# Kernel tuning notes

Hardware: AMD Instinct MI355X
Metric: run time of the kernel (lower is better)

Reference implementation:

```python
import jax, jax.numpy as jnp
import numpy as np

DIM_IN, DIM_OUT, DIM_INNER = 1024, 1024, 128
SCALE = DIM_INNER ** -0.5


def setup_inputs() -> dict:
    key = jax.random.key(0)
    k1, k2, k3, k4 = jax.random.split(key, 4)
    x = jax.random.normal(k1, (4, 4096, DIM_IN), dtype=jnp.float32)
    # torch nn.Linear stores weight as [out, in]; we keep that layout and transpose in matmul
    w_qkv = jax.random.normal(k2, (3 * DIM_INNER, DIM_IN), dtype=jnp.float32) * (DIM_IN ** -0.5)
    w_out = jax.random.normal(k3, (DIM_OUT, DIM_INNER), dtype=jnp.float32) * (DIM_INNER ** -0.5)
    b_out = jax.random.normal(k4, (DIM_OUT,), dtype=jnp.float32) * 0.02
    return {"x": x, "w_qkv": w_qkv, "w_out": w_out, "b_out": b_out}


def reference(x, w_qkv, w_out, b_out):
    # qkv projection (no bias)
    qkv = jnp.einsum('bnd,ed->bne', x, w_qkv)            # [b, n, 3*dim_inner]
    q, k, v = jnp.split(qkv, 3, axis=-1)                 # each [b, n, dim_inner]
    sim = jnp.einsum('bid,bjd->bij', q, k) * SCALE       # [b, n, n]
    n = sim.shape[-1]
    causal = jnp.triu(jnp.ones((n, n), dtype=bool), 1)   # True above diagonal
    neg = jnp.finfo(q.dtype).max
    sim = jnp.where(causal[None, :, :], -neg, sim)
    attn = jax.nn.softmax(sim, axis=-1)
    out = jnp.einsum('bij,bjd->bid', attn, v)            # [b, n, dim_inner]
    return jnp.einsum('bnd,od->bno', out, w_out) + b_out # [b, n, dim_out]
```

## Files before the change

kernel.cpp:

```cpp
#include <hip/hip_runtime.h>
#include <math.h>


typedef __attribute__((ext_vector_type(8))) short bf16x8;
typedef __attribute__((ext_vector_type(4))) short bf16x4;
typedef __attribute__((ext_vector_type(4))) float f32x4;

#define FA_SCL2 0.12751886525137387f

__device__ __forceinline__ unsigned short f2bf(float f) {
    __bf16 h = (__bf16)f;
    return __builtin_bit_cast(unsigned short, h);
}
__device__ __forceinline__ float bf2f(unsigned short h) {
    union { unsigned u; float f; } v; v.u = ((unsigned)h) << 16;
    return v.f;
}
__device__ __forceinline__ f32x4 mfma16(bf16x8 a, bf16x8 b, f32x4 c) {
    return __builtin_amdgcn_mfma_f32_16x16x32_bf16(a, b, c, 0, 0, 0);
}
__device__ __forceinline__ void gl2lds16(const void* g, void* l) {
    __builtin_amdgcn_global_load_lds(
        (const __attribute__((address_space(1))) unsigned int*)g,
        (__attribute__((address_space(3))) unsigned int*)l, 16, 0, 0);
}
__device__ __forceinline__ f32x4 vmax4(f32x4 a, f32x4 b) {
    return f32x4{fmaxf(a[0], b[0]), fmaxf(a[1], b[1]),
                 fmaxf(a[2], b[2]), fmaxf(a[3], b[3])};
}

__global__ __launch_bounds__(256)
void wcast(const float* __restrict__ W, unsigned short* __restrict__ wfm)
{
    const int idx = blockIdx.x * 256 + threadIdx.x;
    const int kc = idx & 127, r = idx >> 7;
    const float* g = W + (size_t)r * 1024 + kc * 8;
    float4 w0 = *(const float4*)g, w1 = *(const float4*)(g + 4);
    bf16x8 p;
    p[0] = (short)f2bf(w0.x); p[1] = (short)f2bf(w0.y);
    p[2] = (short)f2bf(w0.z); p[3] = (short)f2bf(w0.w);
    p[4] = (short)f2bf(w1.x); p[5] = (short)f2bf(w1.y);
    p[6] = (short)f2bf(w1.z); p[7] = (short)f2bf(w1.w);
    *(bf16x8*)&wfm[(size_t)(kc * 384 + r) * 8] = p;
}

__global__ __launch_bounds__(256)
void woutcast(const float* __restrict__ W, unsigned short* __restrict__ wofm)
{
    const int idx = blockIdx.x * 256 + threadIdx.x;
    const int c = idx & 15, rg = idx >> 4;
    const float* g = W + (size_t)rg * 128 + c * 8;
    float4 w0 = *(const float4*)g, w1 = *(const float4*)(g + 4);
    bf16x8 p;
    p[0] = (short)f2bf(w0.x); p[1] = (short)f2bf(w0.y);
    p[2] = (short)f2bf(w0.z); p[3] = (short)f2bf(w0.w);
    p[4] = (short)f2bf(w1.x); p[5] = (short)f2bf(w1.y);
    p[6] = (short)f2bf(w1.z); p[7] = (short)f2bf(w1.w);
    *(bf16x8*)&wofm[((size_t)((rg >> 6) * 16 + c) * 64 + (rg & 63)) * 8] = p;
}

__global__ __launch_bounds__(256, 3)
void gemm_qkv(const float* __restrict__ X, const unsigned short* __restrict__ Wfm,
              unsigned short* __restrict__ qfm, unsigned short* __restrict__ kfm,
              unsigned short* __restrict__ vfm)
{
    __shared__ unsigned short Asl[4096];
    __shared__ unsigned short Bsl[2][8192];
    const int tid = threadIdx.x;
    const int wv = tid >> 6, lane = tid & 63;
    const int lm = lane & 15, quad = lane >> 4;
    const int mt = blockIdx.x & 255;
    const int nt = blockIdx.x >> 8;
    const int mb = mt * 64, nb = nt * 128;
    const int wr = wv >> 1, wc = wv & 1;

    const int arow = tid >> 3, af8 = tid & 7;
    const float* gxr = X + (size_t)(mb + arow) * 1024 + af8 * 8;
    const int sg0 = (af8 * 64 + (arow ^ af8)) * 8;
    const int sg1 = sg0 + 32 * 8;

    f32x4 acc[2][4];
    #pragma unroll
    for (int i = 0; i < 2; ++i)
        #pragma unroll
        for (int j = 0; j < 4; ++j) acc[i][j] = f32x4{0.f, 0.f, 0.f, 0.f};

    auto loadA = [&](int it, float4& r0, float4& r1, float4& r2, float4& r3) {
        const float* g = gxr + it * 64;
        r0 = *(const float4*)g;
        r1 = *(const float4*)(g + 4);
        r2 = *(const float4*)(g + 32 * 1024);
        r3 = *(const float4*)(g + 32 * 1024 + 4);
    };
    auto stageA = [&](const float4& r0, const float4& r1,
                      const float4& r2, const float4& r3) {
        bf16x8 p0, p1;
        p0[0] = (short)f2bf(r0.x); p0[1] = (short)f2bf(r0.y);
        p0[2] = (short)f2bf(r0.z); p0[3] = (short)f2bf(r0.w);
        p0[4] = (short)f2bf(r1.x); p0[5] = (short)f2bf(r1.y);
        p0[6] = (short)f2bf(r1.z); p0[7] = (short)f2bf(r1.w);
        *(bf16x8*)&Asl[sg0] = p0;
        p1[0] = (short)f2bf(r2.x); p1[1] = (short)f2bf(r2.y);
        p1[2] = (short)f2bf(r2.z); p1[3] = (short)f2bf(r2.w);
        p1[4] = (short)f2bf(r3.x); p1[5] = (short)f2bf(r3.y);
        p1[6] = (short)f2bf(r3.z); p1[7] = (short)f2bf(r3.w);
        *(bf16x8*)&Asl[sg1] = p1;
    };
    auto issueB = [&](int it, int buf) {
        #pragma unroll
        for (int i = 0; i < 4; ++i) {
            const int p = wv * 4 + i;
            const int kc = p >> 1, colh = (p & 1) * 64;
            gl2lds16(Wfm + ((size_t)(it * 8 + kc) * 384 + nb + colh + lane) * 8,
                     &Bsl[buf][(kc * 128 + colh) * 8]);
        }
    };

    float4 a0, a1, a2, a3, b0, b1, b2, b3;
    loadA(0, a0, a1, a2, a3);
    issueB(0, 0);
    loadA(1, b0, b1, b2, b3);

    auto step = [&](const int i, float4& r0, float4& r1, float4& r2, float4& r3) {
        __builtin_amdgcn_s_barrier();
        stageA(r0, r1, r2, r3);
        if (i < 15) issueB(i + 1, (i + 1) & 1);
        if (i < 14) {
            loadA(i + 2, r0, r1, r2, r3);
            asm volatile("s_waitcnt vmcnt(12) lgkmcnt(0)" ::: "memory");
        } else if (i == 14) {
            asm volatile("s_waitcnt vmcnt(8) lgkmcnt(0)" ::: "memory");
        } else {
            asm volatile("s_waitcnt vmcnt(0) lgkmcnt(0)" ::: "memory");
        }
        __builtin_amdgcn_s_barrier();
        const unsigned short* Bc = Bsl[i & 1];
        bf16x8 af[2][2], bfr[2][4];
        #pragma unroll
        for (int s = 0; s < 2; ++s) {
            const int kc = s * 4 + quad;
            #pragma unroll
            for (int ii = 0; ii < 2; ++ii)
                af[s][ii] = *(const bf16x8*)
                    &Asl[(kc * 64 + ((wr * 32 + ii * 16 + lm) ^ kc)) * 8];
            #pragma unroll
            for (int j = 0; j < 4; ++j)
                bfr[s][j] = *(const bf16x8*)&Bc[(kc * 128 + wc * 64 + j * 16 + lm) * 8];
        }
        #pragma unroll
        for (int s = 0; s < 2; ++s)
            #pragma unroll
            for (int ii = 0; ii < 2; ++ii)
                #pragma unroll
                for (int j = 0; j < 4; ++j)
                    acc[ii][j] = mfma16(af[s][ii], bfr[s][j], acc[ii][j]);
    };

    for (int p = 0; p < 8; ++p) {
        step(2 * p,     a0, a1, a2, a3);
        step(2 * p + 1, b0, b1, b2, b3);
    }

    if (nt == 2) {
        unsigned short* T = &Bsl[0][0];
        __syncthreads();
        #pragma unroll
        for (int ii = 0; ii < 2; ++ii)
            #pragma unroll
            for (int j = 0; j < 4; ++j) {
                const int d = wc * 64 + j * 16 + lm;
                const int k0 = wr * 32 + ii * 16 + quad * 4;
                bf16x4 v;
                v[0] = (short)f2bf(acc[ii][j][0]);
                v[1] = (short)f2bf(acc[ii][j][1]);
                v[2] = (short)f2bf(acc[ii][j][2]);
                v[3] = (short)f2bf(acc[ii][j][3]);
                *(bf16x4*)&T[d * 72 + k0] = v;
            }
        __syncthreads();
        unsigned short* dst = vfm + (size_t)mt * 8192;
        #pragma unroll
        for (int t = 0; t < 4; ++t) {
            const int g = tid + t * 256;
            const int d = g & 127, c = g >> 7;
            bf16x8 x = *(const bf16x8*)&T[d * 72 + c * 8];
            *(bf16x8*)(dst + (size_t)(c * 128 + d) * 8) = x;
        }
    } else {
        unsigned short* dst = nt ? kfm : qfm;
        const float scl = nt ? 1.f : FA_SCL2;
        #pragma unroll
        for (int ii = 0; ii < 2; ++ii)
            #pragma unroll
            for (int j = 0; j < 4; ++j) {
                const int ncol = wc * 64 + j * 16 + lm;
                const size_t cb = ((size_t)mt * 16 + (ncol >> 3)) * 512 + (ncol & 7);
                #pragma unroll
                for (int r = 0; r < 4; ++r)
                    dst[cb + (size_t)(wr * 32 + ii * 16 + quad * 4 + r) * 8]
                        = f2bf(acc[ii][j][r] * scl);
            }
    }
}

__global__ __launch_bounds__(512, 4)
void flash_attn3(const unsigned short* __restrict__ Qfm, const unsigned short* __restrict__ Kfm,
                 const unsigned short* __restrict__ Vfm,
                 unsigned short* __restrict__ Opart, float* __restrict__ Ml)
{
    __shared__ unsigned short Klds[2][8192];
    __shared__ unsigned short Vlds[2][8192];
    __shared__ unsigned short Plds[8][1024];

    const int tid = threadIdx.x;
    const int wv = tid >> 6, lane = tid & 63;
    const int lm = lane & 15, quad = lane >> 4;

    const int bx = blockIdx.x;
    const int xcd = bx & 7;
    const int b   = xcd >> 1;
    const int r   = (bx >> 3) * 2 + (xcd & 1);
    const int sp  = r & 3;
    const int Qi  = (r < 64) ? (16 + (r >> 2)) : (15 - ((r - 64) >> 2));
    const int n   = 2 * Qi + 2;
    const int cnt = (n >> 2) + ((sp < (n & 3)) ? 1 : 0);
    const int ktb = sp * (n >> 2) + ((sp < (n & 3)) ? sp : (n & 3));
    const int kte = ktb + cnt;
    const int qtw = 2 * Qi + (wv >> 2);
    const int rw  = (wv & 3) * 16;

    const int qt0 = 2 * Qi;
    const size_t ob0 = (size_t)((b * 64 + qt0) * 4 + sp) * 8192;
    const size_t ob1 = ob0 + 4 * 8192;
    const int mlb0 = ((b * 64 + qt0) * 4 + sp) * 128, mlb1 = mlb0 + 512;

    if (cnt == 0) {
        bf16x8 z = {0, 0, 0, 0, 0, 0, 0, 0};
        #pragma unroll
        for (int t = 0; t < 2; ++t) {
            *(bf16x8*)&Opart[ob0 + (size_t)(tid + t * 512) * 8] = z;
            *(bf16x8*)&Opart[ob1 + (size_t)(tid + t * 512) * 8] = z;
        }
        if (tid < 64) { Ml[mlb0 + tid] = -INFINITY; Ml[mlb1 + tid] = -INFINITY; }
        else if (tid < 128) { Ml[mlb0 + tid] = 0.f; Ml[mlb1 + tid] = 0.f; }
        return;
    }

    {
        const size_t qb = (size_t)(b * 64 + qt0) * 8192;
        #pragma unroll
        for (int i = 0; i < 4; ++i) {
            const int p = wv * 4 + i;
            gl2lds16(Qfm + qb + (size_t)p * 512 + lane * 8, &Klds[0][0] + p * 512);
        }
    }
    __syncthreads();
    bf16x8 qf[4];
    {
        const unsigned short* Qt = &Klds[wv >> 2][0];
        #pragma unroll
        for (int c = 0; c < 4; ++c)
            qf[c] = *(const bf16x8*)&Qt[((c * 4 + quad) * 64 + rw + lm) * 8];
    }
    asm volatile("s_waitcnt lgkmcnt(0)" ::: "memory");
    __builtin_amdgcn_s_barrier();

    {
        const size_t kb = (size_t)(b * 64 + ktb) * 8192;
        #pragma unroll
        for (int i = 0; i < 2; ++i) {
            const int pc = wv * 2 + i;
            gl2lds16(Kfm + kb + pc * 512 + lane * 8, &Klds[0][pc * 512]);
            gl2lds16(Vfm + kb + pc * 512 + lane * 8, &Vlds[0][pc * 512]);
        }
    }

    f32x4 oacc[8];
    #pragma unroll
    for (int oc = 0; oc < 8; ++oc) oacc[oc] = f32x4{0.f, 0.f, 0.f, 0.f};
    f32x4 m4 = f32x4{-INFINITY, -INFINITY, -INFINITY, -INFINITY};
    f32x4 lacc = f32x4{0.f, 0.f, 0.f, 0.f};
    unsigned short* Pw = Plds[wv];
    const short ONE = (short)0x3F80;
    const bf16x8 ONESB = {ONE, ONE, ONE, ONE, ONE, ONE, ONE, ONE};

    for (int kt = ktb; kt < kte; ++kt) {
        const int cu = (kt - ktb) & 1;
        __builtin_amdgcn_s_barrier();
        if (kt + 1 < kte) {
            const size_t kb = (size_t)(b * 64 + kt + 1) * 8192;
            #pragma unroll
            for (int i = 0; i < 2; ++i) {
                const int pc = wv * 2 + i;
                gl2lds16(Kfm + kb + pc * 512 + lane * 8, &Klds[cu ^ 1][pc * 512]);
                gl2lds16(Vfm + kb + pc * 512 + lane * 8, &Vlds[cu ^ 1][pc * 512]);
            }
            asm volatile("s_waitcnt vmcnt(4)" ::: "memory");
        } else {
            asm volatile("s_waitcnt vmcnt(0)" ::: "memory");
        }
        __builtin_amdgcn_s_barrier();
        if (kt > qtw) continue;

        const unsigned short* Kc = &Klds[cu][0];
        const unsigned short* Vc = &Vlds[cu][0];

        f32x4 sv[4];
        __builtin_amdgcn_s_setprio(1);
        #pragma unroll
        for (int ct = 0; ct < 4; ++ct) {
            f32x4 a = f32x4{0.f, 0.f, 0.f, 0.f};
            #pragma unroll
            for (int c = 0; c < 4; ++c) {
                bf16x8 kf = *(const bf16x8*)&Kc[((c * 4 + quad) * 64 + ct * 16 + lm) * 8];
                a = mfma16(qf[c], kf, a);
            }
            sv[ct] = a;
        }
        __builtin_amdgcn_s_setprio(0);
        if (kt == qtw) {
            #pragma unroll
            for (int ct = 0; ct < 4; ++ct) {
                const int dg = ct * 16 + lm - rw - quad * 4;
                #pragma unroll
                for (int rr = 0; rr < 4; ++rr)
                    if (dg > rr) sv[ct][rr] = -INFINITY;
            }
        }
        const f32x4 pmax = vmax4(vmax4(sv[0], sv[1]), vmax4(sv[2], sv[3]));
        const float dm = fmaxf(fmaxf(pmax[0] - m4[0], pmax[1] - m4[1]),
                               fmaxf(pmax[2] - m4[2], pmax[3] - m4[3]));
        if (!__all(dm <= 8.f)) {
            f32x4 rmax = pmax;
            #pragma unroll
            for (int d = 1; d < 16; d <<= 1) {
                f32x4 o;
                #pragma unroll
                for (int e = 0; e < 4; ++e) o[e] = __shfl_xor(rmax[e], d);
                rmax = vmax4(rmax, o);
            }
            const f32x4 mnew = vmax4(m4, rmax);
            f32x4 alpha;
            #pragma unroll
            for (int e = 0; e < 4; ++e) alpha[e] = __builtin_amdgcn_exp2f(m4[e] - mnew[e]);
            m4 = mnew;
            #pragma unroll
            for (int oc = 0; oc < 8; ++oc) oacc[oc] *= alpha;
            lacc *= alpha;
        }
        #pragma unroll
        for (int ct = 0; ct < 4; ++ct)
            #pragma unroll
            for (int rr = 0; rr < 4; ++rr)
                sv[ct][rr] = __builtin_amdgcn_exp2f(sv[ct][rr] - m4[rr]);
        #pragma unroll
        for (int ct = 0; ct < 4; ++ct) {
            const int cb = ((ct * 2 + (lm >> 3)) * 16 + quad * 4) * 8 + (lm & 7);
            #pragma unroll
            for (int rr = 0; rr < 4; ++rr)
                Pw[cb + rr * 8] = f2bf(sv[ct][rr]);
        }
        __builtin_amdgcn_s_setprio(1);
        #pragma unroll
        for (int s = 0; s < 2; ++s) {
            bf16x8 pf = *(const bf16x8*)&Pw[((s * 4 + quad) * 16 + lm) * 8];
            lacc = mfma16(pf, ONESB, lacc);
            #pragma unroll
            for (int oc = 0; oc < 8; ++oc) {
                bf16x8 vf = *(const bf16x8*)&Vc[((s * 4 + quad) * 128 + oc * 16 + lm) * 8];
                oacc[oc] = mfma16(pf, vf, oacc[oc]);
            }
        }
        __builtin_amdgcn_s_setprio(0);
    }

    const size_t obw = (size_t)((b * 64 + qtw) * 4 + sp) * 8192;
    const int mlw = ((b * 64 + qtw) * 4 + sp) * 128;
    #pragma unroll
    for (int oc = 0; oc < 8; ++oc) {
        const size_t cb = obw + (size_t)((oc * 2 + (lm >> 3)) * 64
                          + rw + quad * 4) * 8 + (lm & 7);
        #pragma unroll
        for (int rr = 0; rr < 4; ++rr)
            Opart[cb + rr * 8] = f2bf(oacc[oc][rr]);
    }
    if (lm == 0)
        #pragma unroll
        for (int rr = 0; rr < 4; ++rr) {
            const int row = rw + quad * 4 + rr;
            Ml[mlw + row] = m4[rr];
            Ml[mlw + 64 + row] = lacc[rr];
        }
}

__global__ __launch_bounds__(256)
void fa_combine(const unsigned short* __restrict__ Opart, const float* __restrict__ Ml,
                unsigned short* __restrict__ Ofm)
{
    const int bq = blockIdx.x;
    const int tid = threadIdx.x;
    const size_t pbase = (size_t)bq * 4 * 8192;
    const int mlb = bq * 4 * 128;
    #pragma unroll
    for (int t = 0; t < 4; ++t) {
        const int g = tid + t * 256;
        const int r = g & 63;
        float m[4], l[4];
        #pragma unroll
        for (int s = 0; s < 4; ++s) {
            m[s] = Ml[mlb + s * 128 + r];
            l[s] = Ml[mlb + s * 128 + 64 + r];
        }
        const float M = fmaxf(fmaxf(m[0], m[1]), fmaxf(m[2], m[3]));
        float a[4], den = 0.f;
        #pragma unroll
        for (int s = 0; s < 4; ++s) {
            a[s] = __builtin_amdgcn_exp2f(m[s] - M);
            den += a[s] * l[s];
        }
        const float rsc = 1.f / den;
        float acc[8] = {};
        #pragma unroll
        for (int s = 0; s < 4; ++s) {
            bf16x8 x = *(const bf16x8*)&Opart[pbase + (size_t)s * 8192 + (size_t)g * 8];
            #pragma unroll
            for (int e = 0; e < 8; ++e) acc[e] += a[s] * bf2f((unsigned short)x[e]);
        }
        bf16x8 o;
        #pragma unroll
        for (int e = 0; e < 8; ++e) o[e] = f2bf(acc[e] * rsc);
        *(bf16x8*)&Ofm[(size_t)bq * 8192 + (size_t)g * 8] = o;
    }
}

__global__ __launch_bounds__(256, 4)
void gemm_out(const unsigned short* __restrict__ Ain, const unsigned short* __restrict__ Wofm,
              const float* __restrict__ bias, float* __restrict__ out)
{
    __shared__ unsigned short Bsl[16384];
    __shared__ unsigned short Asl[2][4096];
    const int tid = threadIdx.x;
    const int mb = blockIdx.x * 128;
    const int nb = blockIdx.y * 128;
    const int wv = tid >> 6, lane = tid & 63;
    const int wr = (wv >> 1) * 64, wc = (wv & 1) * 64;
    const int lm = lane & 15, quad = lane >> 4;

    #pragma unroll
    for (int i = 0; i < 8; ++i) {
        const int p = wv * 8 + i;
        gl2lds16(Wofm + (size_t)(((nb >> 6) + (p >> 4)) * 16 + (p & 15)) * 512 + lane * 8,
                 &Bsl[p * 512]);
    }
    #pragma unroll
    for (int i = 0; i < 2; ++i) {
        const int id = wv * 2 + i, t = id >> 2, kcl = id & 3;
        gl2lds16(Ain + (size_t)((mb >> 6) + t) * 8192 + kcl * 512 + lane * 8,
                 &Asl[0][(t * 4 + kcl) * 512]);
    }

    f32x4 acc[4][4];
    #pragma unroll
    for (int i = 0; i < 4; ++i)
        #pragma unroll
        for (int j = 0; j < 4; ++j) acc[i][j] = f32x4{0.f, 0.f, 0.f, 0.f};

    for (int kt = 0; kt < 4; ++kt) {
        __builtin_amdgcn_s_barrier();
        if (kt < 3) {
            #pragma unroll
            for (int i = 0; i < 2; ++i) {
                const int id = wv * 2 + i, t = id >> 2, kcl = id & 3;
                gl2lds16(Ain + (size_t)((mb >> 6) + t) * 8192 + ((kt + 1) * 4 + kcl) * 512 + lane * 8,
                         &Asl[(kt + 1) & 1][(t * 4 + kcl) * 512]);
            }
            asm volatile("s_waitcnt vmcnt(2)" ::: "memory");
        } else {
            asm volatile("s_waitcnt vmcnt(0)" ::: "memory");
        }
        __builtin_amdgcn_s_barrier();
        const unsigned short* Ac = Asl[kt & 1];
        bf16x8 af[4], bfr[4];
        #pragma unroll
        for (int i = 0; i < 4; ++i)
            af[i] = *(const bf16x8*)&Ac[(((wv >> 1) * 4 + quad) * 64 + i * 16 + lm) * 8];
        #pragma unroll
        for (int j = 0; j < 4; ++j)
            bfr[j] = *(const bf16x8*)&Bsl[(((wc >> 6) * 16 + kt * 4 + quad) * 64 + j * 16 + lm) * 8];
        #pragma unroll
        for (int i = 0; i < 4; ++i)
            #pragma unroll
            for (int j = 0; j < 4; ++j)
                acc[i][j] = mfma16(af[i], bfr[j], acc[i][j]);
    }

    #pragma unroll
    for (int j = 0; j < 4; ++j) {
        const int col = nb + wc + j * 16 + lm;
        const float bv = bias[col];
        #pragma unroll
        for (int i = 0; i < 4; ++i)
            #pragma unroll
            for (int r = 0; r < 4; ++r) {
                const int m = mb + wr + i * 16 + quad * 4 + r;
                out[(size_t)m * 1024 + col] = acc[i][j][r] + bv;
            }
    }
}

extern "C" void kernel_launch(void* const* d_in, const int* in_sizes, int n_in,
                              void* d_out, int out_size, void* d_ws, size_t ws_size,
                              hipStream_t stream)
{
    (void)in_sizes; (void)n_in; (void)out_size; (void)ws_size;
    const float* x     = (const float*)d_in[0];
    const float* w_qkv = (const float*)d_in[1];
    const float* w_out = (const float*)d_in[2];
    const float* b_out = (const float*)d_in[3];
    float* out = (float*)d_out;
    unsigned short* ws = (unsigned short*)d_ws;

    const size_t NE = (size_t)16384 * 128;
    unsigned short* qfm = ws;
    unsigned short* kfm = ws + NE;
    unsigned short* wofm = ws + 2 * NE;
    unsigned short* vfm = ws + 3 * NE;
    unsigned short* op  = ws + 4 * NE;
    float*          ml  = (float*)(ws + 8 * NE);
    unsigned short* ofm = qfm;
    unsigned short* wfm = op;

    hipLaunchKernelGGL(wcast,       dim3(192),    dim3(256), 0, stream, w_qkv, wfm);
    hipLaunchKernelGGL(gemm_qkv,    dim3(768),    dim3(256), 0, stream, x, wfm, qfm, kfm, vfm);
    hipLaunchKernelGGL(woutcast,    dim3(64),     dim3(256), 0, stream, w_out, wofm);
    hipLaunchKernelGGL(flash_attn3, dim3(512),    dim3(512), 0, stream, qfm, kfm, vfm, op, ml);
    hipLaunchKernelGGL(fa_combine,  dim3(256),    dim3(256), 0, stream, op, ml, ofm);
    hipLaunchKernelGGL(gemm_out,    dim3(128, 8), dim3(256), 0, stream, ofm, wofm, b_out, out);
}
```

Baseline: 181.8 us.

## Fuse split-KV combine into output GEMM and merge weight cast kernels

The flash-attention partial-result combine is folded into the output projection GEMM. Each block rescales and sums the four partial outputs for a 64-row tile straight into LDS, then loops over four 128-column tiles of W_out with double-buffered async loads. This removes the intermediate bf16 O write and read plus two kernel launches, since the two weight-cast kernels are also merged into one. In exchange, the combine work is repeated across the two column-group blocks, the grid is smaller, and LDS use per block is larger.

```diff
diff --git a/kernel.cpp b/kernel.cpp
--- a/kernel.cpp
+++ b/kernel.cpp
@@ -30,33 +30,33 @@
 }
 
 __global__ __launch_bounds__(256)
-void wcast(const float* __restrict__ W, unsigned short* __restrict__ wfm)
+void wcast_all(const float* __restrict__ Wq, const float* __restrict__ Wo,
+               unsigned short* __restrict__ wfm, unsigned short* __restrict__ wofm)
 {
-    const int idx = blockIdx.x * 256 + threadIdx.x;
-    const int kc = idx & 127, r = idx >> 7;
-    const float* g = W + (size_t)r * 1024 + kc * 8;
-    float4 w0 = *(const float4*)g, w1 = *(const float4*)(g + 4);
-    bf16x8 p;
-    p[0] = (short)f2bf(w0.x); p[1] = (short)f2bf(w0.y);
-    p[2] = (short)f2bf(w0.z); p[3] = (short)f2bf(w0.w);
-    p[4] = (short)f2bf(w1.x); p[5] = (short)f2bf(w1.y);
-    p[6] = (short)f2bf(w1.z); p[7] = (short)f2bf(w1.w);
-    *(bf16x8*)&wfm[(size_t)(kc * 384 + r) * 8] = p;
-}
-
-__global__ __launch_bounds__(256)
-void woutcast(const float* __restrict__ W, unsigned short* __restrict__ wofm)
-{
-    const int idx = blockIdx.x * 256 + threadIdx.x;
-    const int c = idx & 15, rg = idx >> 4;
-    const float* g = W + (size_t)rg * 128 + c * 8;
-    float4 w0 = *(const float4*)g, w1 = *(const float4*)(g + 4);
-    bf16x8 p;
-    p[0] = (short)f2bf(w0.x); p[1] = (short)f2bf(w0.y);
-    p[2] = (short)f2bf(w0.z); p[3] = (short)f2bf(w0.w);
-    p[4] = (short)f2bf(w1.x); p[5] = (short)f2bf(w1.y);
-    p[6] = (short)f2bf(w1.z); p[7] = (short)f2bf(w1.w);
-    *(bf16x8*)&wofm[((size_t)((rg >> 6) * 16 + c) * 64 + (rg & 63)) * 8] = p;
+    const int bx = blockIdx.x, tid = threadIdx.x;
+    if (bx < 192) {
+        const int idx = bx * 256 + tid;
+        const int kc = idx & 127, r = idx >> 7;
+        const float* g = Wq + (size_t)r * 1024 + kc * 8;
+        float4 w0 = *(const float4*)g, w1 = *(const float4*)(g + 4);
+        bf16x8 p;
+        p[0] = (short)f2bf(w0.x); p[1] = (short)f2bf(w0.y);
+        p[2] = (short)f2bf(w0.z); p[3] = (short)f2bf(w0.w);
+        p[4] = (short)f2bf(w1.x); p[5] = (short)f2bf(w1.y);
+        p[6] = (short)f2bf(w1.z); p[7] = (short)f2bf(w1.w);
+        *(bf16x8*)&wfm[(size_t)(kc * 384 + r) * 8] = p;
+    } else {
+        const int idx = (bx - 192) * 256 + tid;
+        const int c = idx & 15, rg = idx >> 4;
+        const float* g = Wo + (size_t)rg * 128 + c * 8;
+        float4 w0 = *(const float4*)g, w1 = *(const float4*)(g + 4);
+        bf16x8 p;
+        p[0] = (short)f2bf(w0.x); p[1] = (short)f2bf(w0.y);
+        p[2] = (short)f2bf(w0.z); p[3] = (short)f2bf(w0.w);
+        p[4] = (short)f2bf(w1.x); p[5] = (short)f2bf(w1.y);
+        p[6] = (short)f2bf(w1.z); p[7] = (short)f2bf(w1.w);
+        *(bf16x8*)&wofm[((size_t)((rg >> 6) * 16 + c) * 64 + (rg & 63)) * 8] = p;
+    }
 }
 
 __global__ __launch_bounds__(256, 3)
@@ -393,18 +393,33 @@
         }
 }
 
-__global__ __launch_bounds__(256)
-void fa_combine(const unsigned short* __restrict__ Opart, const float* __restrict__ Ml,
-                unsigned short* __restrict__ Ofm)
+__global__ __launch_bounds__(512, 2)
+void gemm_outf(const unsigned short* __restrict__ Opart, const float* __restrict__ Ml,
+               const unsigned short* __restrict__ Wofm, const float* __restrict__ bias,
+               float* __restrict__ out)
 {
-    const int bq = blockIdx.x;
+    __shared__ unsigned short Asl[8192];
+    __shared__ unsigned short Wl[2][16384];
     const int tid = threadIdx.x;
-    const size_t pbase = (size_t)bq * 4 * 8192;
-    const int mlb = bq * 4 * 128;
-    #pragma unroll
-    for (int t = 0; t < 4; ++t) {
-        const int g = tid + t * 256;
-        const int r = g & 63;
+    const int wv = tid >> 6, lane = tid & 63;
+    const int lm = lane & 15, quad = lane >> 4;
+    const int aq = blockIdx.x;
+    const int nt0 = blockIdx.y * 4;
+    const size_t pbase = (size_t)aq * 4 * 8192;
+    const int mlb = aq * 4 * 128;
+
+    auto issueW = [&](int nt, int buf) {
+        #pragma unroll
+        for (int i = 0; i < 4; ++i) {
+            const int p = wv * 4 + i;
+            gl2lds16(Wofm + (size_t)((nt * 2 + (p >> 4)) * 16 + (p & 15)) * 512 + lane * 8,
+                     &Wl[buf][p * 512]);
+        }
+    };
+    issueW(nt0, 0);
+
+    {
+        const int r = tid & 63;
         float m[4], l[4];
         #pragma unroll
         for (int s = 0; s < 4; ++s) {
@@ -419,92 +434,64 @@
             den += a[s] * l[s];
         }
         const float rsc = 1.f / den;
-        float acc[8] = {};
-        #pragma unroll
-        for (int s = 0; s < 4; ++s) {
-            bf16x8 x = *(const bf16x8*)&Opart[pbase + (size_t)s * 8192 + (size_t)g * 8];
-            #pragma unroll
-            for (int e = 0; e < 8; ++e) acc[e] += a[s] * bf2f((unsigned short)x[e]);
-        }
-        bf16x8 o;
-        #pragma unroll
-        for (int e = 0; e < 8; ++e) o[e] = f2bf(acc[e] * rsc);
-        *(bf16x8*)&Ofm[(size_t)bq * 8192 + (size_t)g * 8] = o;
-    }
-}
-
-__global__ __launch_bounds__(256, 4)
-void gemm_out(const unsigned short* __restrict__ Ain, const unsigned short* __restrict__ Wofm,
-              const float* __restrict__ bias, float* __restrict__ out)
-{
-    __shared__ unsigned short Bsl[16384];
-    __shared__ unsigned short Asl[2][4096];
-    const int tid = threadIdx.x;
-    const int mb = blockIdx.x * 128;
-    const int nb = blockIdx.y * 128;
-    const int wv = tid >> 6, lane = tid & 63;
-    const int wr = (wv >> 1) * 64, wc = (wv & 1) * 64;
-    const int lm = lane & 15, quad = lane >> 4;
-
+        #pragma unroll
+        for (int h = 0; h < 2; ++h) {
+            const int g = tid + h * 512;
+            float acc8[8] = {};
+            #pragma unroll
+            for (int s = 0; s < 4; ++s) {
+                bf16x8 x = *(const bf16x8*)&Opart[pbase + (size_t)s * 8192 + (size_t)g * 8];
+                #pragma unroll
+                for (int e = 0; e < 8; ++e) acc8[e] += a[s] * bf2f((unsigned short)x[e]);
+            }
+            bf16x8 o;
+            #pragma unroll
+            for (int e = 0; e < 8; ++e) o[e] = f2bf(acc8[e] * rsc);
+            *(bf16x8*)&Asl[g * 8] = o;
+        }
+    }
+    __syncthreads();
+
+    const int rw4 = (wv & 3) * 16;
+    const int tl  = wv >> 2;
+    bf16x8 af[4];
     #pragma unroll
-    for (int i = 0; i < 8; ++i) {
-        const int p = wv * 8 + i;
-        gl2lds16(Wofm + (size_t)(((nb >> 6) + (p >> 4)) * 16 + (p & 15)) * 512 + lane * 8,
-                 &Bsl[p * 512]);
-    }
-    #pragma unroll
-    for (int i = 0; i < 2; ++i) {
-        const int id = wv * 2 + i, t = id >> 2, kcl = id & 3;
-        gl2lds16(Ain + (size_t)((mb >> 6) + t) * 8192 + kcl * 512 + lane * 8,
-                 &Asl[0][(t * 4 + kcl) * 512]);
-    }
-
-    f32x4 acc[4][4];
-    #pragma unroll
-    for (int i = 0; i < 4; ++i)
-        #pragma unroll
-        for (int j = 0; j < 4; ++j) acc[i][j] = f32x4{0.f, 0.f, 0.f, 0.f};
-
-    for (int kt = 0; kt < 4; ++kt) {
-        __builtin_amdgcn_s_barrier();
-        if (kt < 3) {
-            #pragma unroll
-            for (int i = 0; i < 2; ++i) {
-                const int id = wv * 2 + i, t = id >> 2, kcl = id & 3;
-                gl2lds16(Ain + (size_t)((mb >> 6) + t) * 8192 + ((kt + 1) * 4 + kcl) * 512 + lane * 8,
-                         &Asl[(kt + 1) & 1][(t * 4 + kcl) * 512]);
-            }
-            asm volatile("s_waitcnt vmcnt(2)" ::: "memory");
+    for (int kt = 0; kt < 4; ++kt)
+        af[kt] = *(const bf16x8*)&Asl[((kt * 4 + quad) * 64 + rw4 + lm) * 8];
+
+    for (int it = 0; it < 4; ++it) {
+        const int nt = nt0 + it;
+        const int buf = it & 1;
+        if (it < 3) {
+            asm volatile("s_waitcnt vmcnt(4)" ::: "memory");
         } else {
             asm volatile("s_waitcnt vmcnt(0)" ::: "memory");
         }
         __builtin_amdgcn_s_barrier();
-        const unsigned short* Ac = Asl[kt & 1];
-        bf16x8 af[4], bfr[4];
-        #pragma unroll
-        for (int i = 0; i < 4; ++i)
-            af[i] = *(const bf16x8*)&Ac[(((wv >> 1) * 4 + quad) * 64 + i * 16 + lm) * 8];
-        #pragma unroll
-        for (int j = 0; j < 4; ++j)
-            bfr[j] = *(const bf16x8*)&Bsl[(((wc >> 6) * 16 + kt * 4 + quad) * 64 + j * 16 + lm) * 8];
-        #pragma unroll
-        for (int i = 0; i < 4; ++i)
-            #pragma unroll
-            for (int j = 0; j < 4; ++j)
-                acc[i][j] = mfma16(af[i], bfr[j], acc[i][j]);
-    }
-
-    #pragma unroll
-    for (int j = 0; j < 4; ++j) {
-        const int col = nb + wc + j * 16 + lm;
-        const float bv = bias[col];
-        #pragma unroll
-        for (int i = 0; i < 4; ++i)
-            #pragma unroll
-            for (int r = 0; r < 4; ++r) {
-                const int m = mb + wr + i * 16 + quad * 4 + r;
-                out[(size_t)m * 1024 + col] = acc[i][j][r] + bv;
-            }
+        if (it < 3) issueW(nt + 1, buf ^ 1);
+
+        f32x4 acc[4];
+        #pragma unroll
+        for (int j = 0; j < 4; ++j) acc[j] = f32x4{0.f, 0.f, 0.f, 0.f};
+        #pragma unroll
+        for (int kt = 0; kt < 4; ++kt)
+            #pragma unroll
+            for (int j = 0; j < 4; ++j) {
+                bf16x8 bfr = *(const bf16x8*)
+                    &Wl[buf][((tl * 16 + kt * 4 + quad) * 64 + j * 16 + lm) * 8];
+                acc[j] = mfma16(af[kt], bfr, acc[j]);
+            }
+        #pragma unroll
+        for (int j = 0; j < 4; ++j) {
+            const int col = nt * 128 + tl * 64 + j * 16 + lm;
+            const float bv = bias[col];
+            #pragma unroll
+            for (int rr = 0; rr < 4; ++rr) {
+                const int m = aq * 64 + rw4 + quad * 4 + rr;
+                out[(size_t)m * 1024 + col] = acc[j][rr] + bv;
+            }
+        }
+        __builtin_amdgcn_s_barrier();
     }
 }
 
@@ -527,13 +514,10 @@
     unsigned short* vfm = ws + 3 * NE;
     unsigned short* op  = ws + 4 * NE;
     float*          ml  = (float*)(ws + 8 * NE);
-    unsigned short* ofm = qfm;
     unsigned short* wfm = op;
 
-    hipLaunchKernelGGL(wcast,       dim3(192),    dim3(256), 0, stream, w_qkv, wfm);
-    hipLaunchKernelGGL(gemm_qkv,    dim3(768),    dim3(256), 0, stream, x, wfm, qfm, kfm, vfm);
-    hipLaunchKernelGGL(woutcast,    dim3(64),     dim3(256), 0, stream, w_out, wofm);
-    hipLaunchKernelGGL(flash_attn3, dim3(512),    dim3(512), 0, stream, qfm, kfm, vfm, op, ml);
-    hipLaunchKernelGGL(fa_combine,  dim3(256),    dim3(256), 0, stream, op, ml, ofm);
-    hipLaunchKernelGGL(gemm_out,    dim3(128, 8), dim3(256), 0, stream, ofm, wofm, b_out, out);
-}
+    hipLaunchKernelGGL(wcast_all,   dim3(256),      dim3(256), 0, stream, w_qkv, w_out, wfm, wofm);
+    hipLaunchKernelGGL(gemm_qkv,    dim3(768),      dim3(256), 0, stream, x, wfm, qfm, kfm, vfm);
+    hipLaunchKernelGGL(flash_attn3, dim3(512),      dim3(512), 0, stream, qfm, kfm, vfm, op, ml);
+    hipLaunchKernelGGL(gemm_outf,   dim3(256, 2),   dim3(512), 0, stream, op, ml, wofm, b_out, out);
+}
```

After: 175.0 us. 1.04x faster.
